# Kernel optimization log

Hardware: AMD Instinct MI355X
Metric: run time of the kernel (lower is better)

Reference implementation:

```python
import jax, jax.numpy as jnp
import numpy as np

NG, NR, C = 50000, 12000, 128     # lane nodes, roi nodes, n_map
NS = 6                            # num_scales
EPS, ELR, E1, E2 = 50000, 5000, 150000, 150000
GN_EPS = 1e-5


def gn(x, sb):
    # GroupNorm(num_groups=1) on [N, C]: normalize over C per row (biased var)
    m = x.mean(-1, keepdims=True)
    v = x.var(-1, keepdims=True)
    return (x - m) / jnp.sqrt(v + GN_EPS) * sb[0] + sb[1]


def lane_pooling(ctx_feat, ctx_pose, tgt_feat, tgt_pose, hi, wi,
                 input_w, relpose_w, relpose_b, ctx1_w, ctx1_gn, ctx2_w,
                 mlp1_w, mlp1_gn, mlp2_w, mlp2_gn, norm_gn):
    dist_feat = jax.nn.relu((ctx_pose[hi] - tgt_pose[wi]) @ relpose_w.T + relpose_b)  # [E,128]
    ctx = jnp.concatenate([ctx_feat[hi], dist_feat], -1)                               # [E,256]
    ctx = jax.nn.relu(gn(ctx @ ctx1_w.T, ctx1_gn)) @ ctx2_w.T                          # [E,128]
    identity = tgt_feat
    t = tgt_feat @ input_w.T
    t = t.at[wi].add(ctx)                 # scatter-reduce onto target nodes
    t = jax.nn.relu(gn(t, norm_gn))
    t = jax.nn.relu(gn(t @ mlp1_w.T, mlp1_gn))
    t = gn(t @ mlp2_w.T, mlp2_gn)
    return jax.nn.relu(t + identity)


def global_graph(feat, ps_u, ps_v, lr_u, lr_v,
                 ctr_w, ps_w, left_w, right_w, norm_gn, ctr2_w, ctr2_gn):
    res = feat
    for i in range(4):  # 4 fusion layers (structurally distinct weights)
        temp = feat @ ctr_w[i].T
        for k in range(2 * NS):  # pre0..pre5, suc0..suc5
            temp = temp.at[ps_u[k]].add(feat[ps_v[k]] @ ps_w[i, k].T)
        temp = temp.at[lr_u[0]].add(feat[lr_v[0]] @ left_w[i].T)
        temp = temp.at[lr_u[1]].add(feat[lr_v[1]] @ right_w[i].T)
        feat = jax.nn.relu(gn(temp, norm_gn[i]))
        feat = gn(feat @ ctr2_w[i].T, ctr2_gn[i])
        feat = jax.nn.relu(feat + res)
        res = feat
    return feat


def _gn_pack(key, lead):
    k1, k2 = jax.random.split(key)
    scale = 1.0 + 0.1 * jax.random.normal(k1, lead + (C,), jnp.float32)
    bias = 0.1 * jax.random.normal(k2, lead + (C,), jnp.float32)
    return jnp.stack([scale, bias], axis=-2)  # [..., 2, C]


def setup_inputs() -> dict:
    key = jax.random.key(0)
    ks = jax.random.split(key, 32)
    w = lambda k, sh: 0.05 * jax.random.normal(k, sh, jnp.float32)
    inp = {
        'roi_feat': jax.random.normal(ks[0], (NR, C), jnp.float32),
        'graph_pose': jax.random.normal(ks[1], (NG, 4), jnp.float32),
        'roi_pose': jax.random.normal(ks[2], (NR, 4), jnp.float32),
        'lp_input_w': w(ks[3], (2, C, C)),
        'lp_relpose_w': w(ks[4], (2, C, 4)),
        'lp_relpose_b': w(ks[5], (2, C)),
        'lp_ctx1_w': w(ks[6], (2, C, 2 * C)),
        'lp_ctx1_gn': _gn_pack(ks[7], (2,)),
        'lp_ctx2_w': w(ks[8], (2, C, C)),
        'lp_mlp1_w': w(ks[9], (2, C, C)),
        'lp_mlp1_gn': _gn_pack(ks[10], (2,)),
        'lp_mlp2_w': w(ks[11], (2, C, C)),
        'lp_mlp2_gn': _gn_pack(ks[12], (2,)),
        'lp_norm_gn': _gn_pack(ks[13], (2,)),
        'fuse_ctr_w': w(ks[14], (4, C, C)),
        'fuse_ps_w': w(ks[15], (4, 2 * NS, C, C)),
        'fuse_left_w': w(ks[16], (4, C, C)),
        'fuse_right_w': w(ks[17], (4, C, C)),
        'fuse_norm_gn': _gn_pack(ks[18], (4,)),
        'fuse_ctr2_w': w(ks[19], (4, C, C)),
        'fuse_ctr2_gn': _gn_pack(ks[20], (4,)),
        'e1_hi': jax.random.randint(ks[21], (E1,), 0, NR, jnp.int32),
        'e1_wi': jax.random.randint(ks[22], (E1,), 0, NG, jnp.int32),
        'e2_hi': jax.random.randint(ks[23], (E2,), 0, NG, jnp.int32),
        'e2_wi': jax.random.randint(ks[24], (E2,), 0, NR, jnp.int32),
        'ps_u': jax.random.randint(ks[25], (2 * NS, EPS), 0, NG, jnp.int32),
        'ps_v': jax.random.randint(ks[26], (2 * NS, EPS), 0, NG, jnp.int32),
        'lr_u': jax.random.randint(ks[27], (2, ELR), 0, NG, jnp.int32),
        'lr_v': jax.random.randint(ks[28], (2, ELR), 0, NG, jnp.int32),
    }
    return inp


def reference(roi_feat, graph_pose, roi_pose, lp_input_w, lp_relpose_w, lp_relpose_b,
              lp_ctx1_w, lp_ctx1_gn, lp_ctx2_w, lp_mlp1_w, lp_mlp1_gn, lp_mlp2_w,
              lp_mlp2_gn, lp_norm_gn, fuse_ctr_w, fuse_ps_w, fuse_left_w, fuse_right_w,
              fuse_norm_gn, fuse_ctr2_w, fuse_ctr2_gn, e1_hi, e1_wi, e2_hi, e2_wi,
              ps_u, ps_v, lr_u, lr_v):
    lp = lambda j: (lp_input_w[j], lp_relpose_w[j], lp_relpose_b[j], lp_ctx1_w[j],
                    lp_ctx1_gn[j], lp_ctx2_w[j], lp_mlp1_w[j], lp_mlp1_gn[j],
                    lp_mlp2_w[j], lp_mlp2_gn[j], lp_norm_gn[j])
    graph_feat = jnp.zeros((NG, C), jnp.float32)
    # roi2graph: context = roi, target = graph
    graph_feat = lane_pooling(roi_feat, roi_pose, graph_feat, graph_pose, e1_hi, e1_wi, *lp(0))
    graph_feat = global_graph(graph_feat, ps_u, ps_v, lr_u, lr_v,
                              fuse_ctr_w, fuse_ps_w, fuse_left_w, fuse_right_w,
                              fuse_norm_gn, fuse_ctr2_w, fuse_ctr2_gn)
    # graph2roi: context = graph, target = roi
    out = lane_pooling(graph_feat, graph_pose, roi_feat, roi_pose, e2_hi, e2_wi, *lp(1))
    return out
```

## Files before the change

### kernel.cpp

```cpp
#include <hip/hip_runtime.h>

#define NG 50000
#define NR 12000
#define EPS_N 50000
#define ELR_N 5000
#define E1_N 150000
#define E2_N 150000
#define GN_EPS_F 1e-5f
#define SCAN_CHUNK 4096
#define AST 136

typedef __attribute__((ext_vector_type(8))) __bf16 bf16x8;
typedef __attribute__((ext_vector_type(4))) float f32x4;

__device__ __forceinline__ bf16x8 cvt8(const float* __restrict__ p) {
    float4 x0 = *reinterpret_cast<const float4*>(p);
    float4 x1 = *reinterpret_cast<const float4*>(p + 4);
    bf16x8 a;
    a[0] = (__bf16)x0.x; a[1] = (__bf16)x0.y; a[2] = (__bf16)x0.z; a[3] = (__bf16)x0.w;
    a[4] = (__bf16)x1.x; a[5] = (__bf16)x1.y; a[6] = (__bf16)x1.z; a[7] = (__bf16)x1.w;
    return a;
}

struct PrepTab { const float* src[80]; int stride[80]; int n; };

__global__ void prepw_k(PrepTab tab, __bf16* __restrict__ wbuf)
{
    int t = blockIdx.x * 256 + threadIdx.x;
    int w = t >> 11;
    if (w >= tab.n) return;
    int rr = t & 2047;
    int chunk = rr >> 6, l = rr & 63;
    int waveN = chunk >> 4, ks = (chunk >> 2) & 3, ni = chunk & 3;
    int c = waveN * 64 + ni * 16 + (l & 15);
    int kb = (ks * 4 + (l >> 4)) * 8;
    const float* s = tab.src[w] + (size_t)c * tab.stride[w] + kb;
    bf16x8 o;
    #pragma unroll
    for (int e = 0; e < 8; ++e) o[e] = (__bf16)s[e];
    *reinterpret_cast<bf16x8*>(wbuf + (size_t)w * 16384 + rr * 8) = o;
}

__global__ void hist14_k(const int* __restrict__ ps_u, const int* __restrict__ lr_u,
                         int* __restrict__ cnt)
{
    int t = blockIdx.x * 256 + threadIdx.x;
    const int total = 12 * EPS_N + 2 * ELR_N;
    if (t >= total) return;
    int k, u;
    if (t < 12 * EPS_N) { k = t / EPS_N; u = ps_u[t]; }
    else { int r = t - 12 * EPS_N; k = 12 + r / ELR_N; u = lr_u[r]; }
    atomicAdd(&cnt[k * NG + u], 1);
}

__global__ void fill14_k(const int* __restrict__ ps_u, const int* __restrict__ ps_v,
                         const int* __restrict__ lr_u, const int* __restrict__ lr_v,
                         int* __restrict__ head, int* __restrict__ col)
{
    int t = blockIdx.x * 256 + threadIdx.x;
    const int total = 12 * EPS_N + 2 * ELR_N;
    if (t >= total) return;
    int k, u, v;
    if (t < 12 * EPS_N) { k = t / EPS_N; u = ps_u[t]; v = ps_v[t]; }
    else { int r = t - 12 * EPS_N; k = 12 + r / ELR_N; u = lr_u[r]; v = lr_v[r]; }
    int pos = atomicAdd(&head[k * NG + u], 1);
    col[pos] = v;
}

__global__ void histE_k(const int* __restrict__ wi, int n, int* __restrict__ cnt)
{
    int t = blockIdx.x * 256 + threadIdx.x;
    if (t >= n) return;
    atomicAdd(&cnt[wi[t]], 1);
}

__global__ void fillE_k(const int* __restrict__ wi, int n,
                        int* __restrict__ head, int* __restrict__ col)
{
    int t = blockIdx.x * 256 + threadIdx.x;
    if (t >= n) return;
    int pos = atomicAdd(&head[wi[t]], 1);
    col[pos] = t;
}

__global__ void scan1_k(const int* __restrict__ in, int n, int* __restrict__ bsum)
{
    __shared__ int sm[4];
    int base = blockIdx.x * SCAN_CHUNK;
    int s = 0;
    for (int i = threadIdx.x; i < SCAN_CHUNK; i += 256) {
        int idx = base + i;
        s += (idx < n) ? in[idx] : 0;
    }
    #pragma unroll
    for (int off = 1; off < 64; off <<= 1) s += __shfl_xor(s, off);
    if ((threadIdx.x & 63) == 0) sm[threadIdx.x >> 6] = s;
    __syncthreads();
    if (threadIdx.x == 0) bsum[blockIdx.x] = sm[0] + sm[1] + sm[2] + sm[3];
}

__global__ void scan2_k(int* __restrict__ bsum, int nb)
{
    if (threadIdx.x == 0) {
        int acc = 0;
        for (int i = 0; i < nb; ++i) { int t = bsum[i]; bsum[i] = acc; acc += t; }
    }
}

__global__ void scan3_k(const int* __restrict__ in, int n,
                        const int* __restrict__ bsum, int* __restrict__ outp)
{
    __shared__ int sm[256];
    int base = blockIdx.x * SCAN_CHUNK;
    int loc[16]; int s = 0;
    #pragma unroll
    for (int i = 0; i < 16; ++i) {
        int idx = base + threadIdx.x * 16 + i;
        loc[i] = (idx < n) ? in[idx] : 0; s += loc[i];
    }
    sm[threadIdx.x] = s; __syncthreads();
    for (int off = 1; off < 256; off <<= 1) {
        int v = (threadIdx.x >= off) ? sm[threadIdx.x - off] : 0;
        __syncthreads();
        sm[threadIdx.x] += v;
        __syncthreads();
    }
    int tp = (threadIdx.x ? sm[threadIdx.x - 1] : 0) + bsum[blockIdx.x];
    #pragma unroll
    for (int i = 0; i < 16; ++i) {
        int idx = base + threadIdx.x * 16 + i;
        if (idx < n) outp[idx] = tp;
        tp += loc[i];
        if (idx == n - 1) outp[n] = tp;
    }
}

__device__ __forceinline__ void mfma_tile(f32x4 (&acc)[2][4], const __bf16* atile,
                                          const __bf16* __restrict__ gw,
                                          int waveN, int r16, int kq, int lane)
{
    const __bf16* gwb = gw + ((size_t)waveN << 13) + lane * 8;
    #pragma unroll
    for (int ks = 0; ks < 4; ++ks) {
        bf16x8 a[2], b[4];
        #pragma unroll
        for (int mi = 0; mi < 2; ++mi) {
            const int lr = mi * 16 + r16;
            a[mi] = *reinterpret_cast<const bf16x8*>(atile + lr * AST + ((ks << 2) + kq) * 8);
        }
        #pragma unroll
        for (int ni = 0; ni < 4; ++ni)
            b[ni] = *reinterpret_cast<const bf16x8*>(gwb + ((ks << 2) + ni) * 512);
        #pragma unroll
        for (int mi = 0; mi < 2; ++mi)
            #pragma unroll
            for (int ni = 0; ni < 4; ++ni)
                acc[mi][ni] = __builtin_amdgcn_mfma_f32_16x16x32_bf16(
                    a[mi], b[ni], acc[mi][ni], 0, 0, 0);
    }
}

__device__ __forceinline__ void gn_stats(const f32x4 (&acc)[2][4],
                                         float (*smS)[32], float (*smQ)[32],
                                         int waveN, int r16, int kq)
{
    #pragma unroll
    for (int mi = 0; mi < 2; ++mi) {
        #pragma unroll
        for (int reg = 0; reg < 4; ++reg) {
            float s = acc[mi][0][reg] + acc[mi][1][reg] + acc[mi][2][reg] + acc[mi][3][reg];
            float q = acc[mi][0][reg]*acc[mi][0][reg] + acc[mi][1][reg]*acc[mi][1][reg]
                    + acc[mi][2][reg]*acc[mi][2][reg] + acc[mi][3][reg]*acc[mi][3][reg];
            #pragma unroll
            for (int off = 1; off < 16; off <<= 1) {
                s += __shfl_xor(s, off);
                q += __shfl_xor(q, off);
            }
            if (r16 == 0) {
                int lr = mi * 16 + kq * 4 + reg;
                smS[waveN][lr] = s; smQ[waveN][lr] = q;
            }
        }
    }
}

template<typename CT>
__launch_bounds__(128, 3)
__global__ void edgefull_k(const int* __restrict__ hi_idx, const int* __restrict__ wi_idx,
                           const CT* __restrict__ ctxfeat,
                           const float* __restrict__ cpose, const float* __restrict__ tpose,
                           const float* __restrict__ rpw, const float* __restrict__ rpb,
                           const __bf16* __restrict__ wc1A, const __bf16* __restrict__ wc1B,
                           const float* __restrict__ sb,
                           __bf16* __restrict__ hout, int M)
{
    __shared__ __bf16 atile[32 * AST];
    __shared__ float rw[640];
    __shared__ float smS[2][32], smQ[2][32];
    const int tid = threadIdx.x, lane = tid & 63, waveN = tid >> 6;
    const int r16 = lane & 15, kq = lane >> 4;
    const int ublk = blockIdx.x * 32;

    for (int i = tid; i < 640; i += 128)
        rw[i] = (i < 512) ? rpw[i] : rpb[i - 512];

    float dl[2][4];
    #pragma unroll
    for (int mi = 0; mi < 2; ++mi) {
        int r = ublk + mi * 16 + r16;
        int e = r < M ? r : M - 1;
        int hi = hi_idx[e], wi = wi_idx[e];
        float4 cp = *reinterpret_cast<const float4*>(cpose + (size_t)hi * 4);
        float4 tp = *reinterpret_cast<const float4*>(tpose + (size_t)wi * 4);
        dl[mi][0] = cp.x - tp.x; dl[mi][1] = cp.y - tp.y;
        dl[mi][2] = cp.z - tp.z; dl[mi][3] = cp.w - tp.w;
    }

    {
        const int glr = tid >> 2, q = tid & 3;
        const int e = (ublk + glr) < M ? (ublk + glr) : M - 1;
        const int cr = hi_idx[e];
        const CT* sp = ctxfeat + (size_t)cr * 128 + q * 32;
        #pragma unroll
        for (int i = 0; i < 4; ++i) {
            bf16x8 h;
            if constexpr (sizeof(CT) == 4) h = cvt8((const float*)sp + i * 8);
            else h = *reinterpret_cast<const bf16x8*>((const __bf16*)sp + i * 8);
            *reinterpret_cast<bf16x8*>(atile + glr * AST + (q * 4 + i) * 8) = h;
        }
    }
    __syncthreads();

    f32x4 acc[2][4];
    #pragma unroll
    for (int mi = 0; mi < 2; ++mi)
        #pragma unroll
        for (int ni = 0; ni < 4; ++ni)
            acc[mi][ni] = (f32x4){0.f, 0.f, 0.f, 0.f};

    mfma_tile(acc, atile, wc1A, waveN, r16, kq, lane);

    {
        const __bf16* gwb = wc1B + ((size_t)waveN << 13) + lane * 8;
        #pragma unroll
        for (int ks = 0; ks < 4; ++ks) {
            bf16x8 a[2], b[4];
            #pragma unroll
            for (int mi = 0; mi < 2; ++mi) {
                #pragma unroll
                for (int i = 0; i < 8; ++i) {
                    const int k = ks * 32 + kq * 8 + i;
                    float4 w4 = *reinterpret_cast<const float4*>(&rw[k * 4]);
                    float d = fmaf(dl[mi][0], w4.x, fmaf(dl[mi][1], w4.y,
                              fmaf(dl[mi][2], w4.z, fmaf(dl[mi][3], w4.w, rw[512 + k]))));
                    a[mi][i] = (__bf16)fmaxf(d, 0.f);
                }
            }
            #pragma unroll
            for (int ni = 0; ni < 4; ++ni)
                b[ni] = *reinterpret_cast<const bf16x8*>(gwb + ((ks << 2) + ni) * 512);
            #pragma unroll
            for (int mi = 0; mi < 2; ++mi)
                #pragma unroll
                for (int ni = 0; ni < 4; ++ni)
                    acc[mi][ni] = __builtin_amdgcn_mfma_f32_16x16x32_bf16(
                        a[mi], b[ni], acc[mi][ni], 0, 0, 0);
        }
    }

    gn_stats(acc, smS, smQ, waveN, r16, kq);
    __syncthreads();

    #pragma unroll
    for (int mi = 0; mi < 2; ++mi) {
        #pragma unroll
        for (int reg = 0; reg < 4; ++reg) {
            const int lr = mi * 16 + kq * 4 + reg;
            const float S = smS[0][lr] + smS[1][lr];
            const float Q = smQ[0][lr] + smQ[1][lr];
            const float m = S * (1.f / 128.f);
            const float inv = rsqrtf(fmaxf(Q * (1.f / 128.f) - m * m, 0.f) + GN_EPS_F);
            const int crow = ublk + lr;
            if (crow < M) {
                __bf16* dp = hout + (size_t)crow * 128 + waveN * 64 + r16;
                #pragma unroll
                for (int ni = 0; ni < 4; ++ni) {
                    const int colc = waveN * 64 + ni * 16 + r16;
                    float y = (acc[mi][ni][reg] - m) * inv * sb[colc] + sb[128 + colc];
                    dp[ni * 16] = (__bf16)fmaxf(y, 0.f);
                }
            }
        }
    }
}

struct FW { const __bf16* w[16]; };

__launch_bounds__(128, 3)
__global__ void fusedlayer_k(const __bf16* __restrict__ feat,
                             const int* __restrict__ rp, const int* __restrict__ col,
                             FW fw, const float* __restrict__ gn1,
                             const float* __restrict__ gn2,
                             __bf16* __restrict__ outp, int M)
{
    __shared__ __bf16 atile[2][32 * AST];
    __shared__ float smS[2][32], smQ[2][32];
    const int tid = threadIdx.x, lane = tid & 63, waveN = tid >> 6;
    const int r16 = lane & 15, kq = lane >> 4;
    const int ublk = blockIdx.x * 32;
    const int glr = tid >> 2, q = tid & 3;
    const int grow = ublk + glr;
    const bool gv = grow < M;
    const int grc = gv ? grow : 0;

    int begs[14], degs[14], c0[14];
    #pragma unroll
    for (int j = 0; j < 14; ++j) {
        int b = 0, e = 0;
        if (gv) { b = rp[j * M + grow]; e = rp[j * M + grow + 1]; }
        begs[j] = b; degs[j] = e - b;
    }
    #pragma unroll
    for (int j = 0; j < 14; ++j)
        c0[j] = (degs[j] > 0) ? col[begs[j]] : 0;

    float ss[32];
    auto GATHER = [&](int jj) {
        #pragma unroll
        for (int i = 0; i < 32; ++i) ss[i] = 0.f;
        if (jj == 14) {
            const __bf16* sp = feat + (size_t)grc * 128 + q * 32;
            #pragma unroll
            for (int i = 0; i < 4; ++i) {
                bf16x8 h = *reinterpret_cast<const bf16x8*>(sp + i * 8);
                #pragma unroll
                for (int e = 0; e < 8; ++e) ss[i * 8 + e] = (float)h[e];
            }
        } else {
            const int d = degs[jj];
            if (d > 0) {
                const __bf16* sp = feat + (size_t)c0[jj] * 128 + q * 32;
                #pragma unroll
                for (int i = 0; i < 4; ++i) {
                    bf16x8 h = *reinterpret_cast<const bf16x8*>(sp + i * 8);
                    #pragma unroll
                    for (int e2 = 0; e2 < 8; ++e2) ss[i * 8 + e2] += (float)h[e2];
                }
            }
            for (int t2 = begs[jj] + 1; t2 < begs[jj] + d; ++t2) {
                const __bf16* sp = feat + (size_t)col[t2] * 128 + q * 32;
                #pragma unroll
                for (int i = 0; i < 4; ++i) {
                    bf16x8 h = *reinterpret_cast<const bf16x8*>(sp + i * 8);
                    #pragma unroll
                    for (int e2 = 0; e2 < 8; ++e2) ss[i * 8 + e2] += (float)h[e2];
                }
            }
        }
    };

    f32x4 acc[2][4];
    #pragma unroll
    for (int mi = 0; mi < 2; ++mi)
        #pragma unroll
        for (int ni = 0; ni < 4; ++ni)
            acc[mi][ni] = (f32x4){0.f, 0.f, 0.f, 0.f};

    GATHER(0);
    #pragma unroll
    for (int j = 0; j < 15; ++j) {
        __bf16* at = atile[j & 1];
        #pragma unroll
        for (int i = 0; i < 4; ++i) {
            bf16x8 o;
            #pragma unroll
            for (int e = 0; e < 8; ++e) o[e] = (__bf16)ss[i * 8 + e];
            *reinterpret_cast<bf16x8*>(at + glr * AST + (q * 4 + i) * 8) = o;
        }
        __syncthreads();
        if (j < 14) GATHER(j + 1);
        mfma_tile(acc, at, fw.w[j], waveN, r16, kq, lane);
    }

    gn_stats(acc, smS, smQ, waveN, r16, kq);
    __syncthreads();
    {
        __bf16* at = atile[1];
        #pragma unroll
        for (int mi = 0; mi < 2; ++mi) {
            #pragma unroll
            for (int reg = 0; reg < 4; ++reg) {
                const int lr = mi * 16 + kq * 4 + reg;
                const float S = smS[0][lr] + smS[1][lr];
                const float Q = smQ[0][lr] + smQ[1][lr];
                const float m = S * (1.f / 128.f);
                const float inv = rsqrtf(fmaxf(Q * (1.f / 128.f) - m * m, 0.f) + GN_EPS_F);
                #pragma unroll
                for (int ni = 0; ni < 4; ++ni) {
                    const int colc = waveN * 64 + ni * 16 + r16;
                    float y = (acc[mi][ni][reg] - m) * inv * gn1[colc] + gn1[128 + colc];
                    at[lr * AST + colc] = (__bf16)fmaxf(y, 0.f);
                }
            }
        }
    }
    __syncthreads();

    f32x4 acc2[2][4];
    #pragma unroll
    for (int mi = 0; mi < 2; ++mi)
        #pragma unroll
        for (int ni = 0; ni < 4; ++ni)
            acc2[mi][ni] = (f32x4){0.f, 0.f, 0.f, 0.f};
    mfma_tile(acc2, atile[1], fw.w[15], waveN, r16, kq, lane);

    gn_stats(acc2, smS, smQ, waveN, r16, kq);
    __syncthreads();
    #pragma unroll
    for (int mi = 0; mi < 2; ++mi) {
        #pragma unroll
        for (int reg = 0; reg < 4; ++reg) {
            const int lr = mi * 16 + kq * 4 + reg;
            const float S = smS[0][lr] + smS[1][lr];
            const float Q = smQ[0][lr] + smQ[1][lr];
            const float m = S * (1.f / 128.f);
            const float inv = rsqrtf(fmaxf(Q * (1.f / 128.f) - m * m, 0.f) + GN_EPS_F);
            const int crow = ublk + lr;
            if (crow < M) {
                __bf16* dp = outp + (size_t)crow * 128 + waveN * 64 + r16;
                const __bf16* rs = feat + (size_t)crow * 128 + waveN * 64 + r16;
                #pragma unroll
                for (int ni = 0; ni < 4; ++ni) {
                    const int colc = waveN * 64 + ni * 16 + r16;
                    float y = (acc2[mi][ni][reg] - m) * inv * gn2[colc] + gn2[128 + colc];
                    y += (float)rs[ni * 16];
                    dp[ni * 16] = (__bf16)fmaxf(y, 0.f);
                }
            }
        }
    }
}

template<bool LP2>
__launch_bounds__(128, 3)
__global__ void lptail_k(const __bf16* __restrict__ hsrc,
                         const int* __restrict__ rp, const int* __restrict__ col,
                         const float* __restrict__ roi,
                         const __bf16* __restrict__ wc2, const __bf16* __restrict__ winW,
                         const __bf16* __restrict__ wm1, const __bf16* __restrict__ wm2,
                         const float* __restrict__ ngn, const float* __restrict__ m1gn,
                         const float* __restrict__ m2gn,
                         void* __restrict__ outp, int M)
{
    __shared__ __bf16 atile[32 * AST];
    __shared__ float smS[2][32], smQ[2][32];
    const int tid = threadIdx.x, lane = tid & 63, waveN = tid >> 6;
    const int r16 = lane & 15, kq = lane >> 4;
    const int ublk = blockIdx.x * 32;
    const int glr = tid >> 2, q = tid & 3;
    const int grow = ublk + glr;
    const bool gv = grow < M;

    {
        float ss[32];
        #pragma unroll
        for (int i = 0; i < 32; ++i) ss[i] = 0.f;
        if (gv) {
            const int b = rp[grow], e = rp[grow + 1];
            for (int jj = b; jj < e; ++jj) {
                const __bf16* sp = hsrc + (size_t)col[jj] * 128 + q * 32;
                #pragma unroll
                for (int i = 0; i < 4; ++i) {
                    bf16x8 h = *reinterpret_cast<const bf16x8*>(sp + i * 8);
                    #pragma unroll
                    for (int e2 = 0; e2 < 8; ++e2) ss[i * 8 + e2] += (float)h[e2];
                }
            }
        }
        #pragma unroll
        for (int i = 0; i < 4; ++i) {
            bf16x8 o;
            #pragma unroll
            for (int e2 = 0; e2 < 8; ++e2) o[e2] = (__bf16)ss[i * 8 + e2];
            *reinterpret_cast<bf16x8*>(atile + glr * AST + (q * 4 + i) * 8) = o;
        }
    }
    __syncthreads();

    f32x4 acc[2][4];
    #pragma unroll
    for (int mi = 0; mi < 2; ++mi)
        #pragma unroll
        for (int ni = 0; ni < 4; ++ni)
            acc[mi][ni] = (f32x4){0.f, 0.f, 0.f, 0.f};
    mfma_tile(acc, atile, wc2, waveN, r16, kq, lane);

    if (LP2) {
        __syncthreads();
        {
            const float* sp = roi + (size_t)(gv ? grow : 0) * 128 + q * 32;
            #pragma unroll
            for (int i = 0; i < 4; ++i)
                *reinterpret_cast<bf16x8*>(atile + glr * AST + (q * 4 + i) * 8) =
                    cvt8(sp + i * 8);
        }
        __syncthreads();
        mfma_tile(acc, atile, winW, waveN, r16, kq, lane);
    }

    auto CHAIN = [&](const float* SBP, const __bf16* WNEXT) {
        gn_stats(acc, smS, smQ, waveN, r16, kq);
        __syncthreads();
        #pragma unroll
        for (int mi = 0; mi < 2; ++mi) {
            #pragma unroll
            for (int reg = 0; reg < 4; ++reg) {
                const int lr = mi * 16 + kq * 4 + reg;
                const float S = smS[0][lr] + smS[1][lr];
                const float Q = smQ[0][lr] + smQ[1][lr];
                const float m = S * (1.f / 128.f);
                const float inv = rsqrtf(fmaxf(Q * (1.f / 128.f) - m * m, 0.f) + GN_EPS_F);
                #pragma unroll
                for (int ni = 0; ni < 4; ++ni) {
                    const int colc = waveN * 64 + ni * 16 + r16;
                    float y = (acc[mi][ni][reg] - m) * inv * SBP[colc] + SBP[128 + colc];
                    atile[lr * AST + colc] = (__bf16)fmaxf(y, 0.f);
                }
            }
        }
        __syncthreads();
        #pragma unroll
        for (int mi = 0; mi < 2; ++mi)
            #pragma unroll
            for (int ni = 0; ni < 4; ++ni)
                acc[mi][ni] = (f32x4){0.f, 0.f, 0.f, 0.f};
        mfma_tile(acc, atile, WNEXT, waveN, r16, kq, lane);
    };
    CHAIN(ngn, wm1);
    CHAIN(m1gn, wm2);

    gn_stats(acc, smS, smQ, waveN, r16, kq);
    __syncthreads();
    #pragma unroll
    for (int mi = 0; mi < 2; ++mi) {
        #pragma unroll
        for (int reg = 0; reg < 4; ++reg) {
            const int lr = mi * 16 + kq * 4 + reg;
            const float S = smS[0][lr] + smS[1][lr];
            const float Q = smQ[0][lr] + smQ[1][lr];
            const float m = S * (1.f / 128.f);
            const float inv = rsqrtf(fmaxf(Q * (1.f / 128.f) - m * m, 0.f) + GN_EPS_F);
            const int crow = ublk + lr;
            if (crow < M) {
                #pragma unroll
                for (int ni = 0; ni < 4; ++ni) {
                    const int colc = waveN * 64 + ni * 16 + r16;
                    float y = (acc[mi][ni][reg] - m) * inv * m2gn[colc] + m2gn[128 + colc];
                    if (LP2) {
                        y += roi[(size_t)crow * 128 + colc];
                        ((float*)outp)[(size_t)crow * 128 + colc] = fmaxf(y, 0.f);
                    } else {
                        ((__bf16*)outp)[(size_t)crow * 128 + colc] = (__bf16)fmaxf(y, 0.f);
                    }
                }
            }
        }
    }
}

extern "C" void kernel_launch(void* const* d_in, const int* in_sizes, int n_in,
                              void* d_out, int out_size, void* d_ws, size_t ws_size,
                              hipStream_t stream)
{
    const float* roi_feat   = (const float*)d_in[0];
    const float* graph_pose = (const float*)d_in[1];
    const float* roi_pose   = (const float*)d_in[2];
    const float* lp_input_w = (const float*)d_in[3];
    const float* lp_rpw     = (const float*)d_in[4];
    const float* lp_rpb     = (const float*)d_in[5];
    const float* lp_c1w     = (const float*)d_in[6];
    const float* lp_c1gn    = (const float*)d_in[7];
    const float* lp_c2w     = (const float*)d_in[8];
    const float* lp_m1w     = (const float*)d_in[9];
    const float* lp_m1gn    = (const float*)d_in[10];
    const float* lp_m2w     = (const float*)d_in[11];
    const float* lp_m2gn    = (const float*)d_in[12];
    const float* lp_ngn     = (const float*)d_in[13];
    const float* f_ctrw     = (const float*)d_in[14];
    const float* f_psw      = (const float*)d_in[15];
    const float* f_lw       = (const float*)d_in[16];
    const float* f_rw       = (const float*)d_in[17];
    const float* f_ngn      = (const float*)d_in[18];
    const float* f_c2w      = (const float*)d_in[19];
    const float* f_c2gn     = (const float*)d_in[20];
    const int* e1_hi = (const int*)d_in[21];
    const int* e1_wi = (const int*)d_in[22];
    const int* e2_hi = (const int*)d_in[23];
    const int* e2_wi = (const int*)d_in[24];
    const int* ps_u  = (const int*)d_in[25];
    const int* ps_v  = (const int*)d_in[26];
    const int* lr_u  = (const int*)d_in[27];
    const int* lr_v  = (const int*)d_in[28];
    float* out = (float*)d_out;

    __bf16* gA   = (__bf16*)d_ws;
    __bf16* gB   = gA + (size_t)NG * 128;
    __bf16* hbuf = gB + (size_t)NG * 128;
    __bf16* wbuf = hbuf + (size_t)E1_N * 128;
    int* ip      = (int*)(wbuf + (size_t)80 * 16384);
    int* cnt14   = ip;             ip += 14 * NG;
    int* rp14    = ip;             ip += 14 * NG + 1;
    int* col14   = ip;             ip += 12 * EPS_N + 2 * ELR_N;
    int* cntE1   = ip;             ip += NG;
    int* rpE1    = ip;             ip += NG + 1;
    int* colE1   = ip;             ip += E1_N;
    int* cntE2   = ip;             ip += NR;
    int* rpE2    = ip;             ip += NR + 1;
    int* colE2   = ip;             ip += E2_N;
    int* bsum    = ip;             ip += 256;

    dim3 blk(256), blk128(128);
    const dim3 gNG32((NG + 31) / 32), gNR32((NR + 31) / 32), gE32((E1_N + 31) / 32);
    const int NE14 = 12 * EPS_N + 2 * ELR_N;
    const dim3 gH14((NE14 + 255) / 256);

    PrepTab tab; int nw = 0;
    auto addw = [&](const float* p, int s) { tab.src[nw] = p; tab.stride[nw] = s; ++nw; };
    addw(lp_c1w, 256);
    addw(lp_c1w + 128, 256);
    addw(lp_c1w + 32768, 256);
    addw(lp_c1w + 32768 + 128, 256);
    addw(lp_input_w + 16384, 128);
    addw(lp_c2w, 128); addw(lp_c2w + 16384, 128);
    addw(lp_m1w, 128); addw(lp_m1w + 16384, 128);
    addw(lp_m2w, 128); addw(lp_m2w + 16384, 128);
    for (int i = 0; i < 4; ++i) addw(f_ctrw + (size_t)i * 16384, 128);
    for (int i = 0; i < 4; ++i)
        for (int k = 0; k < 12; ++k) addw(f_psw + ((size_t)i * 12 + k) * 16384, 128);
    for (int i = 0; i < 4; ++i) addw(f_lw + (size_t)i * 16384, 128);
    for (int i = 0; i < 4; ++i) addw(f_rw + (size_t)i * 16384, 128);
    for (int i = 0; i < 4; ++i) addw(f_c2w + (size_t)i * 16384, 128);
    tab.n = nw;
    auto wb = [&](int idx) { return (const __bf16*)(wbuf + (size_t)idx * 16384); };
    prepw_k<<<dim3((nw * 2048 + 255) / 256), blk, 0, stream>>>(tab, wbuf);

    hipMemsetAsync(cnt14, 0, (size_t)14 * NG * 4, stream);
    hist14_k<<<gH14, blk, 0, stream>>>(ps_u, lr_u, cnt14);
    {
        int n = 14 * NG, nb = (n + SCAN_CHUNK - 1) / SCAN_CHUNK;
        scan1_k<<<nb, blk, 0, stream>>>(cnt14, n, bsum);
        scan2_k<<<1, blk, 0, stream>>>(bsum, nb);
        scan3_k<<<nb, blk, 0, stream>>>(cnt14, n, bsum, rp14);
    }
    hipMemcpyAsync(cnt14, rp14, (size_t)14 * NG * 4, hipMemcpyDeviceToDevice, stream);
    fill14_k<<<gH14, blk, 0, stream>>>(ps_u, ps_v, lr_u, lr_v, cnt14, col14);

    hipMemsetAsync(cntE1, 0, (size_t)NG * 4, stream);
    histE_k<<<(E1_N + 255) / 256, blk, 0, stream>>>(e1_wi, E1_N, cntE1);
    {
        int n = NG, nb = (n + SCAN_CHUNK - 1) / SCAN_CHUNK;
        scan1_k<<<nb, blk, 0, stream>>>(cntE1, n, bsum);
        scan2_k<<<1, blk, 0, stream>>>(bsum, nb);
        scan3_k<<<nb, blk, 0, stream>>>(cntE1, n, bsum, rpE1);
    }
    hipMemcpyAsync(cntE1, rpE1, (size_t)NG * 4, hipMemcpyDeviceToDevice, stream);
    fillE_k<<<(E1_N + 255) / 256, blk, 0, stream>>>(e1_wi, E1_N, cntE1, colE1);

    hipMemsetAsync(cntE2, 0, (size_t)NR * 4, stream);
    histE_k<<<(E2_N + 255) / 256, blk, 0, stream>>>(e2_wi, E2_N, cntE2);
    {
        int n = NR, nb = (n + SCAN_CHUNK - 1) / SCAN_CHUNK;
        scan1_k<<<nb, blk, 0, stream>>>(cntE2, n, bsum);
        scan2_k<<<1, blk, 0, stream>>>(bsum, nb);
        scan3_k<<<nb, blk, 0, stream>>>(cntE2, n, bsum, rpE2);
    }
    hipMemcpyAsync(cntE2, rpE2, (size_t)NR * 4, hipMemcpyDeviceToDevice, stream);
    fillE_k<<<(E2_N + 255) / 256, blk, 0, stream>>>(e2_wi, E2_N, cntE2, colE2);

    edgefull_k<float><<<gE32, blk128, 0, stream>>>(
        e1_hi, e1_wi, roi_feat, roi_pose, graph_pose, lp_rpw, lp_rpb,
        wb(0), wb(1), lp_c1gn, hbuf, E1_N);
    lptail_k<false><<<gNG32, blk128, 0, stream>>>(
        hbuf, rpE1, colE1, nullptr, wb(5), nullptr, wb(7), wb(9),
        lp_ngn, lp_m1gn, lp_m2gn, gA, NG);

    for (int i = 0; i < 4; ++i) {
        FW fw;
        for (int k = 0; k < 12; ++k) fw.w[k] = wb(15 + i * 12 + k);
        fw.w[12] = wb(63 + i); fw.w[13] = wb(67 + i);
        fw.w[14] = wb(11 + i); fw.w[15] = wb(71 + i);
        const __bf16* src = (i & 1) ? gB : gA;
        __bf16* dst = (i & 1) ? gA : gB;
        fusedlayer_k<<<gNG32, blk128, 0, stream>>>(
            src, rp14, col14, fw, f_ngn + (size_t)i * 256,
            f_c2gn + (size_t)i * 256, dst, NG);
    }

    edgefull_k<__bf16><<<gE32, blk128, 0, stream>>>(
        e2_hi, e2_wi, gA, graph_pose, roi_pose, lp_rpw + 512, lp_rpb + 128,
        wb(2), wb(3), lp_c1gn + 256, hbuf, E2_N);
    lptail_k<true><<<gNR32, blk128, 0, stream>>>(
        hbuf, rpE2, colE2, roi_feat, wb(6), wb(4), wb(8), wb(10),
        lp_ngn + 256, lp_m1gn + 256, lp_m2gn + 256, out, NR);
}
```

Measured before the change: 765.1 us.

## Give each wave a full 16x128 output tile and build MFMA fragments in registers

The work split changes from two waves sharing a 32-row tile (each owning 64 columns) to each wave owning 16 rows across all 128 columns. A-fragments are now gathered straight from global memory into registers in MFMA layout, and GroupNorm statistics are reduced within the wave by shuffles. This drops the shared-memory A tile, the cross-wave stat exchange and most block barriers. The cost is twice as many B-weight loads per wave (8 column fragments instead of 4), higher register pressure from 8 accumulators, and the loss of the software-pipelined gather that overlapped the next gather with the current MFMAs in the fusion kernel.

```diff
diff --git a/kernel.cpp b/kernel.cpp
--- a/kernel.cpp
+++ b/kernel.cpp
@@ -8,7 +8,7 @@
 #define E2_N 150000
 #define GN_EPS_F 1e-5f
 #define SCAN_CHUNK 4096
-#define AST 136
+#define WST 136
 
 typedef __attribute__((ext_vector_type(8))) __bf16 bf16x8;
 typedef __attribute__((ext_vector_type(4))) float f32x4;
@@ -31,8 +31,8 @@
     if (w >= tab.n) return;
     int rr = t & 2047;
     int chunk = rr >> 6, l = rr & 63;
-    int waveN = chunk >> 4, ks = (chunk >> 2) & 3, ni = chunk & 3;
-    int c = waveN * 64 + ni * 16 + (l & 15);
+    int wn = chunk >> 4, ks = (chunk >> 2) & 3, ni = chunk & 3;
+    int c = wn * 64 + ni * 16 + (l & 15);
     int kb = (ks * 4 + (l >> 4)) * 8;
     const float* s = tab.src[w] + (size_t)c * tab.stride[w] + kb;
     bf16x8 o;
@@ -135,53 +135,65 @@
     }
 }
 
-__device__ __forceinline__ void mfma_tile(f32x4 (&acc)[2][4], const __bf16* atile,
-                                          const __bf16* __restrict__ gw,
-                                          int waveN, int r16, int kq, int lane)
-{
-    const __bf16* gwb = gw + ((size_t)waveN << 13) + lane * 8;
+
+__device__ __forceinline__ void mfma16(f32x4 (&acc)[8], const bf16x8 (&a)[4],
+                                       const __bf16* __restrict__ gw, int lane)
+{
+    const __bf16* gwb = gw + lane * 8;
     #pragma unroll
     for (int ks = 0; ks < 4; ++ks) {
-        bf16x8 a[2], b[4];
-        #pragma unroll
-        for (int mi = 0; mi < 2; ++mi) {
-            const int lr = mi * 16 + r16;
-            a[mi] = *reinterpret_cast<const bf16x8*>(atile + lr * AST + ((ks << 2) + kq) * 8);
-        }
-        #pragma unroll
-        for (int ni = 0; ni < 4; ++ni)
-            b[ni] = *reinterpret_cast<const bf16x8*>(gwb + ((ks << 2) + ni) * 512);
-        #pragma unroll
-        for (int mi = 0; mi < 2; ++mi)
-            #pragma unroll
-            for (int ni = 0; ni < 4; ++ni)
-                acc[mi][ni] = __builtin_amdgcn_mfma_f32_16x16x32_bf16(
-                    a[mi], b[ni], acc[mi][ni], 0, 0, 0);
-    }
-}
-
-__device__ __forceinline__ void gn_stats(const f32x4 (&acc)[2][4],
-                                         float (*smS)[32], float (*smQ)[32],
-                                         int waveN, int r16, int kq)
-{
-    #pragma unroll
-    for (int mi = 0; mi < 2; ++mi) {
-        #pragma unroll
-        for (int reg = 0; reg < 4; ++reg) {
-            float s = acc[mi][0][reg] + acc[mi][1][reg] + acc[mi][2][reg] + acc[mi][3][reg];
-            float q = acc[mi][0][reg]*acc[mi][0][reg] + acc[mi][1][reg]*acc[mi][1][reg]
-                    + acc[mi][2][reg]*acc[mi][2][reg] + acc[mi][3][reg]*acc[mi][3][reg];
-            #pragma unroll
-            for (int off = 1; off < 16; off <<= 1) {
-                s += __shfl_xor(s, off);
-                q += __shfl_xor(q, off);
-            }
-            if (r16 == 0) {
-                int lr = mi * 16 + kq * 4 + reg;
-                smS[waveN][lr] = s; smQ[waveN][lr] = q;
-            }
-        }
-    }
+        #pragma unroll
+        for (int n2 = 0; n2 < 8; ++n2) {
+            const int chunk = (n2 >> 2) * 16 + ks * 4 + (n2 & 3);
+            bf16x8 b = *reinterpret_cast<const bf16x8*>(gwb + chunk * 512);
+            acc[n2] = __builtin_amdgcn_mfma_f32_16x16x32_bf16(a[ks], b, acc[n2], 0, 0, 0);
+        }
+    }
+}
+
+__device__ __forceinline__ void ss_to_frags(const float (&ss)[32], bf16x8 (&a)[4])
+{
+    #pragma unroll
+    for (int ks = 0; ks < 4; ++ks)
+        #pragma unroll
+        for (int i = 0; i < 8; ++i)
+            a[ks][i] = (__bf16)ss[ks * 8 + i];
+}
+
+__device__ __forceinline__ void gn_mi(const f32x4 (&acc)[8], float (&m)[4], float (&inv)[4])
+{
+    #pragma unroll
+    for (int reg = 0; reg < 4; ++reg) {
+        float s = 0.f, q = 0.f;
+        #pragma unroll
+        for (int n2 = 0; n2 < 8; ++n2) { float v = acc[n2][reg]; s += v; q = fmaf(v, v, q); }
+        #pragma unroll
+        for (int off = 1; off < 16; off <<= 1) {
+            s += __shfl_xor(s, off);
+            q += __shfl_xor(q, off);
+        }
+        m[reg] = s * (1.f / 128.f);
+        inv[reg] = rsqrtf(fmaxf(q * (1.f / 128.f) - m[reg] * m[reg], 0.f) + GN_EPS_F);
+    }
+}
+
+__device__ __forceinline__ void gn_relayout(const f32x4 (&acc)[8], const float* __restrict__ sb,
+                                            __bf16* wl, bf16x8 (&a)[4], int r16, int kq)
+{
+    float m[4], inv[4];
+    gn_mi(acc, m, inv);
+    #pragma unroll
+    for (int reg = 0; reg < 4; ++reg) {
+        #pragma unroll
+        for (int n2 = 0; n2 < 8; ++n2) {
+            const int colc = n2 * 16 + r16;
+            float y = (acc[n2][reg] - m[reg]) * inv[reg] * sb[colc] + sb[128 + colc];
+            wl[(kq * 4 + reg) * WST + colc] = (__bf16)fmaxf(y, 0.f);
+        }
+    }
+    #pragma unroll
+    for (int ks = 0; ks < 4; ++ks)
+        a[ks] = *reinterpret_cast<const bf16x8*>(wl + r16 * WST + ks * 32 + kq * 8);
 }
 
 template<typename CT>
@@ -194,101 +206,63 @@
                            const float* __restrict__ sb,
                            __bf16* __restrict__ hout, int M)
 {
-    __shared__ __bf16 atile[32 * AST];
     __shared__ float rw[640];
-    __shared__ float smS[2][32], smQ[2][32];
-    const int tid = threadIdx.x, lane = tid & 63, waveN = tid >> 6;
+    const int tid = threadIdx.x, lane = tid & 63, wv = tid >> 6;
     const int r16 = lane & 15, kq = lane >> 4;
-    const int ublk = blockIdx.x * 32;
+    const int wbase = blockIdx.x * 32 + wv * 16;
+    const int erow = wbase + r16;
+    const int ec = erow < M ? erow : M - 1;
 
     for (int i = tid; i < 640; i += 128)
         rw[i] = (i < 512) ? rpw[i] : rpb[i - 512];
-
-    float dl[2][4];
-    #pragma unroll
-    for (int mi = 0; mi < 2; ++mi) {
-        int r = ublk + mi * 16 + r16;
-        int e = r < M ? r : M - 1;
-        int hi = hi_idx[e], wi = wi_idx[e];
-        float4 cp = *reinterpret_cast<const float4*>(cpose + (size_t)hi * 4);
-        float4 tp = *reinterpret_cast<const float4*>(tpose + (size_t)wi * 4);
-        dl[mi][0] = cp.x - tp.x; dl[mi][1] = cp.y - tp.y;
-        dl[mi][2] = cp.z - tp.z; dl[mi][3] = cp.w - tp.w;
-    }
-
-    {
-        const int glr = tid >> 2, q = tid & 3;
-        const int e = (ublk + glr) < M ? (ublk + glr) : M - 1;
-        const int cr = hi_idx[e];
-        const CT* sp = ctxfeat + (size_t)cr * 128 + q * 32;
-        #pragma unroll
-        for (int i = 0; i < 4; ++i) {
-            bf16x8 h;
-            if constexpr (sizeof(CT) == 4) h = cvt8((const float*)sp + i * 8);
-            else h = *reinterpret_cast<const bf16x8*>((const __bf16*)sp + i * 8);
-            *reinterpret_cast<bf16x8*>(atile + glr * AST + (q * 4 + i) * 8) = h;
-        }
-    }
     __syncthreads();
 
-    f32x4 acc[2][4];
-    #pragma unroll
-    for (int mi = 0; mi < 2; ++mi)
-        #pragma unroll
-        for (int ni = 0; ni < 4; ++ni)
-            acc[mi][ni] = (f32x4){0.f, 0.f, 0.f, 0.f};
-
-    mfma_tile(acc, atile, wc1A, waveN, r16, kq, lane);
-
-    {
-        const __bf16* gwb = wc1B + ((size_t)waveN << 13) + lane * 8;
+    const int hi = hi_idx[ec], wi = wi_idx[ec];
+    float4 cp = *reinterpret_cast<const float4*>(cpose + (size_t)hi * 4);
+    float4 tp = *reinterpret_cast<const float4*>(tpose + (size_t)wi * 4);
+    const float d0 = cp.x - tp.x, d1 = cp.y - tp.y, d2 = cp.z - tp.z, d3 = cp.w - tp.w;
+
+    f32x4 acc[8];
+    #pragma unroll
+    for (int n2 = 0; n2 < 8; ++n2) acc[n2] = (f32x4){0.f, 0.f, 0.f, 0.f};
+
+    {
+        bf16x8 a[4];
+        const CT* sp = ctxfeat + (size_t)hi * 128 + kq * 8;
         #pragma unroll
         for (int ks = 0; ks < 4; ++ks) {
-            bf16x8 a[2], b[4];
+            if constexpr (sizeof(CT) == 4) a[ks] = cvt8((const float*)sp + ks * 32);
+            else a[ks] = *reinterpret_cast<const bf16x8*>((const __bf16*)sp + ks * 32);
+        }
+        mfma16(acc, a, wc1A, lane);
+    }
+    {
+        bf16x8 a[4];
+        #pragma unroll
+        for (int ks = 0; ks < 4; ++ks)
             #pragma unroll
-            for (int mi = 0; mi < 2; ++mi) {
-                #pragma unroll
-                for (int i = 0; i < 8; ++i) {
-                    const int k = ks * 32 + kq * 8 + i;
-                    float4 w4 = *reinterpret_cast<const float4*>(&rw[k * 4]);
-                    float d = fmaf(dl[mi][0], w4.x, fmaf(dl[mi][1], w4.y,
-                              fmaf(dl[mi][2], w4.z, fmaf(dl[mi][3], w4.w, rw[512 + k]))));
-                    a[mi][i] = (__bf16)fmaxf(d, 0.f);
-                }
-            }
+            for (int i = 0; i < 8; ++i) {
+                const int k = ks * 32 + kq * 8 + i;
+                float4 w4 = *reinterpret_cast<const float4*>(&rw[k * 4]);
+                float d = fmaf(d0, w4.x, fmaf(d1, w4.y, fmaf(d2, w4.z,
+                          fmaf(d3, w4.w, rw[512 + k]))));
+                a[ks][i] = (__bf16)fmaxf(d, 0.f);
+            }
+        mfma16(acc, a, wc1B, lane);
+    }
+
+    float m[4], inv[4];
+    gn_mi(acc, m, inv);
+    #pragma unroll
+    for (int reg = 0; reg < 4; ++reg) {
+        const int crow = wbase + kq * 4 + reg;
+        if (crow < M) {
+            __bf16* dp = hout + (size_t)crow * 128 + r16;
             #pragma unroll
-            for (int ni = 0; ni < 4; ++ni)
-                b[ni] = *reinterpret_cast<const bf16x8*>(gwb + ((ks << 2) + ni) * 512);
-            #pragma unroll
-            for (int mi = 0; mi < 2; ++mi)
-                #pragma unroll
-                for (int ni = 0; ni < 4; ++ni)
-                    acc[mi][ni] = __builtin_amdgcn_mfma_f32_16x16x32_bf16(
-                        a[mi], b[ni], acc[mi][ni], 0, 0, 0);
-        }
-    }
-
-    gn_stats(acc, smS, smQ, waveN, r16, kq);
-    __syncthreads();
-
-    #pragma unroll
-    for (int mi = 0; mi < 2; ++mi) {
-        #pragma unroll
-        for (int reg = 0; reg < 4; ++reg) {
-            const int lr = mi * 16 + kq * 4 + reg;
-            const float S = smS[0][lr] + smS[1][lr];
-            const float Q = smQ[0][lr] + smQ[1][lr];
-            const float m = S * (1.f / 128.f);
-            const float inv = rsqrtf(fmaxf(Q * (1.f / 128.f) - m * m, 0.f) + GN_EPS_F);
-            const int crow = ublk + lr;
-            if (crow < M) {
-                __bf16* dp = hout + (size_t)crow * 128 + waveN * 64 + r16;
-                #pragma unroll
-                for (int ni = 0; ni < 4; ++ni) {
-                    const int colc = waveN * 64 + ni * 16 + r16;
-                    float y = (acc[mi][ni][reg] - m) * inv * sb[colc] + sb[128 + colc];
-                    dp[ni * 16] = (__bf16)fmaxf(y, 0.f);
-                }
+            for (int n2 = 0; n2 < 8; ++n2) {
+                const int colc = n2 * 16 + r16;
+                float y = (acc[n2][reg] - m[reg]) * inv[reg] * sb[colc] + sb[128 + colc];
+                dp[n2 * 16] = (__bf16)fmaxf(y, 0.f);
             }
         }
     }
@@ -303,139 +277,67 @@
                              const float* __restrict__ gn2,
                              __bf16* __restrict__ outp, int M)
 {
-    __shared__ __bf16 atile[2][32 * AST];
-    __shared__ float smS[2][32], smQ[2][32];
-    const int tid = threadIdx.x, lane = tid & 63, waveN = tid >> 6;
+    __shared__ __bf16 wl[2][16 * WST];
+    const int tid = threadIdx.x, lane = tid & 63, wv = tid >> 6;
     const int r16 = lane & 15, kq = lane >> 4;
-    const int ublk = blockIdx.x * 32;
-    const int glr = tid >> 2, q = tid & 3;
-    const int grow = ublk + glr;
-    const bool gv = grow < M;
-    const int grc = gv ? grow : 0;
-
-    int begs[14], degs[14], c0[14];
-    #pragma unroll
-    for (int j = 0; j < 14; ++j) {
-        int b = 0, e = 0;
-        if (gv) { b = rp[j * M + grow]; e = rp[j * M + grow + 1]; }
-        begs[j] = b; degs[j] = e - b;
-    }
-    #pragma unroll
-    for (int j = 0; j < 14; ++j)
-        c0[j] = (degs[j] > 0) ? col[begs[j]] : 0;
-
-    float ss[32];
-    auto GATHER = [&](int jj) {
+    const int wbase = blockIdx.x * 32 + wv * 16;
+    const int wrow = (wbase + r16) < M ? (wbase + r16) : M - 1;
+
+    f32x4 acc[8];
+    #pragma unroll
+    for (int n2 = 0; n2 < 8; ++n2) acc[n2] = (f32x4){0.f, 0.f, 0.f, 0.f};
+
+    #pragma unroll
+    for (int j = 0; j < 15; ++j) {
+        float ss[32];
         #pragma unroll
         for (int i = 0; i < 32; ++i) ss[i] = 0.f;
-        if (jj == 14) {
-            const __bf16* sp = feat + (size_t)grc * 128 + q * 32;
+        if (j == 14) {
+            const __bf16* sp = feat + (size_t)wrow * 128 + kq * 8;
             #pragma unroll
-            for (int i = 0; i < 4; ++i) {
-                bf16x8 h = *reinterpret_cast<const bf16x8*>(sp + i * 8);
+            for (int ks = 0; ks < 4; ++ks) {
+                bf16x8 h = *reinterpret_cast<const bf16x8*>(sp + ks * 32);
                 #pragma unroll
-                for (int e = 0; e < 8; ++e) ss[i * 8 + e] = (float)h[e];
+                for (int i = 0; i < 8; ++i) ss[ks * 8 + i] = (float)h[i];
             }
         } else {
-            const int d = degs[jj];
-            if (d > 0) {
-                const __bf16* sp = feat + (size_t)c0[jj] * 128 + q * 32;
+            const int b = rp[j * M + wrow], e = rp[j * M + wrow + 1];
+            for (int t2 = b; t2 < e; ++t2) {
+                const __bf16* sp = feat + (size_t)col[t2] * 128 + kq * 8;
                 #pragma unroll
-                for (int i = 0; i < 4; ++i) {
-                    bf16x8 h = *reinterpret_cast<const bf16x8*>(sp + i * 8);
+                for (int ks = 0; ks < 4; ++ks) {
+                    bf16x8 h = *reinterpret_cast<const bf16x8*>(sp + ks * 32);
                     #pragma unroll
-                    for (int e2 = 0; e2 < 8; ++e2) ss[i * 8 + e2] += (float)h[e2];
+                    for (int i = 0; i < 8; ++i) ss[ks * 8 + i] += (float)h[i];
                 }
             }
-            for (int t2 = begs[jj] + 1; t2 < begs[jj] + d; ++t2) {
-                const __bf16* sp = feat + (size_t)col[t2] * 128 + q * 32;
-                #pragma unroll
-                for (int i = 0; i < 4; ++i) {
-                    bf16x8 h = *reinterpret_cast<const bf16x8*>(sp + i * 8);
-                    #pragma unroll
-                    for (int e2 = 0; e2 < 8; ++e2) ss[i * 8 + e2] += (float)h[e2];
-                }
-            }
-        }
-    };
-
-    f32x4 acc[2][4];
-    #pragma unroll
-    for (int mi = 0; mi < 2; ++mi)
-        #pragma unroll
-        for (int ni = 0; ni < 4; ++ni)
-            acc[mi][ni] = (f32x4){0.f, 0.f, 0.f, 0.f};
-
-    GATHER(0);
-    #pragma unroll
-    for (int j = 0; j < 15; ++j) {
-        __bf16* at = atile[j & 1];
-        #pragma unroll
-        for (int i = 0; i < 4; ++i) {
-            bf16x8 o;
+        }
+        bf16x8 a[4];
+        ss_to_frags(ss, a);
+        mfma16(acc, a, fw.w[j], lane);
+    }
+
+    bf16x8 a2[4];
+    gn_relayout(acc, gn1, wl[wv], a2, r16, kq);
+    f32x4 acc2[8];
+    #pragma unroll
+    for (int n2 = 0; n2 < 8; ++n2) acc2[n2] = (f32x4){0.f, 0.f, 0.f, 0.f};
+    mfma16(acc2, a2, fw.w[15], lane);
+
+    float m[4], inv[4];
+    gn_mi(acc2, m, inv);
+    #pragma unroll
+    for (int reg = 0; reg < 4; ++reg) {
+        const int crow = wbase + kq * 4 + reg;
+        if (crow < M) {
+            __bf16* dp = outp + (size_t)crow * 128 + r16;
+            const __bf16* rs = feat + (size_t)crow * 128 + r16;
             #pragma unroll
-            for (int e = 0; e < 8; ++e) o[e] = (__bf16)ss[i * 8 + e];
-            *reinterpret_cast<bf16x8*>(at + glr * AST + (q * 4 + i) * 8) = o;
-        }
-        __syncthreads();
-        if (j < 14) GATHER(j + 1);
-        mfma_tile(acc, at, fw.w[j], waveN, r16, kq, lane);
-    }
-
-    gn_stats(acc, smS, smQ, waveN, r16, kq);
-    __syncthreads();
-    {
-        __bf16* at = atile[1];
-        #pragma unroll
-        for (int mi = 0; mi < 2; ++mi) {
-            #pragma unroll
-            for (int reg = 0; reg < 4; ++reg) {
-                const int lr = mi * 16 + kq * 4 + reg;
-                const float S = smS[0][lr] + smS[1][lr];
-                const float Q = smQ[0][lr] + smQ[1][lr];
-                const float m = S * (1.f / 128.f);
-                const float inv = rsqrtf(fmaxf(Q * (1.f / 128.f) - m * m, 0.f) + GN_EPS_F);
-                #pragma unroll
-                for (int ni = 0; ni < 4; ++ni) {
-                    const int colc = waveN * 64 + ni * 16 + r16;
-                    float y = (acc[mi][ni][reg] - m) * inv * gn1[colc] + gn1[128 + colc];
-                    at[lr * AST + colc] = (__bf16)fmaxf(y, 0.f);
-                }
-            }
-        }
-    }
-    __syncthreads();
-
-    f32x4 acc2[2][4];
-    #pragma unroll
-    for (int mi = 0; mi < 2; ++mi)
-        #pragma unroll
-        for (int ni = 0; ni < 4; ++ni)
-            acc2[mi][ni] = (f32x4){0.f, 0.f, 0.f, 0.f};
-    mfma_tile(acc2, atile[1], fw.w[15], waveN, r16, kq, lane);
-
-    gn_stats(acc2, smS, smQ, waveN, r16, kq);
-    __syncthreads();
-    #pragma unroll
-    for (int mi = 0; mi < 2; ++mi) {
-        #pragma unroll
-        for (int reg = 0; reg < 4; ++reg) {
-            const int lr = mi * 16 + kq * 4 + reg;
-            const float S = smS[0][lr] + smS[1][lr];
-            const float Q = smQ[0][lr] + smQ[1][lr];
-            const float m = S * (1.f / 128.f);
-            const float inv = rsqrtf(fmaxf(Q * (1.f / 128.f) - m * m, 0.f) + GN_EPS_F);
-            const int crow = ublk + lr;
-            if (crow < M) {
-                __bf16* dp = outp + (size_t)crow * 128 + waveN * 64 + r16;
-                const __bf16* rs = feat + (size_t)crow * 128 + waveN * 64 + r16;
-                #pragma unroll
-                for (int ni = 0; ni < 4; ++ni) {
-                    const int colc = waveN * 64 + ni * 16 + r16;
-                    float y = (acc2[mi][ni][reg] - m) * inv * gn2[colc] + gn2[128 + colc];
-                    y += (float)rs[ni * 16];
-                    dp[ni * 16] = (__bf16)fmaxf(y, 0.f);
-                }
+            for (int n2 = 0; n2 < 8; ++n2) {
+                const int colc = n2 * 16 + r16;
+                float y = (acc2[n2][reg] - m[reg]) * inv[reg] * gn2[colc] + gn2[128 + colc];
+                y += (float)rs[n2 * 16];
+                dp[n2 * 16] = (__bf16)fmaxf(y, 0.f);
             }
         }
     }
@@ -452,116 +354,72 @@
                          const float* __restrict__ m2gn,
                          void* __restrict__ outp, int M)
 {
-    __shared__ __bf16 atile[32 * AST];
-    __shared__ float smS[2][32], smQ[2][32];
-    const int tid = threadIdx.x, lane = tid & 63, waveN = tid >> 6;
+    __shared__ __bf16 wl[2][16 * WST];
+    const int tid = threadIdx.x, lane = tid & 63, wv = tid >> 6;
     const int r16 = lane & 15, kq = lane >> 4;
-    const int ublk = blockIdx.x * 32;
-    const int glr = tid >> 2, q = tid & 3;
-    const int grow = ublk + glr;
-    const bool gv = grow < M;
+    const int wbase = blockIdx.x * 32 + wv * 16;
+    const int wrow = (wbase + r16) < M ? (wbase + r16) : M - 1;
+
+    f32x4 acc[8];
+    #pragma unroll
+    for (int n2 = 0; n2 < 8; ++n2) acc[n2] = (f32x4){0.f, 0.f, 0.f, 0.f};
 
     {
         float ss[32];
         #pragma unroll
         for (int i = 0; i < 32; ++i) ss[i] = 0.f;
-        if (gv) {
-            const int b = rp[grow], e = rp[grow + 1];
-            for (int jj = b; jj < e; ++jj) {
-                const __bf16* sp = hsrc + (size_t)col[jj] * 128 + q * 32;
+        const int b = rp[wrow], e = rp[wrow + 1];
+        for (int t2 = b; t2 < e; ++t2) {
+            const __bf16* sp = hsrc + (size_t)col[t2] * 128 + kq * 8;
+            #pragma unroll
+            for (int ks = 0; ks < 4; ++ks) {
+                bf16x8 h = *reinterpret_cast<const bf16x8*>(sp + ks * 32);
                 #pragma unroll
-                for (int i = 0; i < 4; ++i) {
-                    bf16x8 h = *reinterpret_cast<const bf16x8*>(sp + i * 8);
-                    #pragma unroll
-                    for (int e2 = 0; e2 < 8; ++e2) ss[i * 8 + e2] += (float)h[e2];
-                }
-            }
-        }
-        #pragma unroll
-        for (int i = 0; i < 4; ++i) {
-            bf16x8 o;
+                for (int i = 0; i < 8; ++i) ss[ks * 8 + i] += (float)h[i];
+            }
+        }
+        bf16x8 a[4];
+        ss_to_frags(ss, a);
+        mfma16(acc, a, wc2, lane);
+    }
+    if (LP2) {
+        bf16x8 a[4];
+        const float* sp = roi + (size_t)wrow * 128 + kq * 8;
+        #pragma unroll
+        for (int ks = 0; ks < 4; ++ks) a[ks] = cvt8(sp + ks * 32);
+        mfma16(acc, a, winW, lane);
+    }
+
+    {
+        bf16x8 a[4];
+        gn_relayout(acc, ngn, wl[wv], a, r16, kq);
+        #pragma unroll
+        for (int n2 = 0; n2 < 8; ++n2) acc[n2] = (f32x4){0.f, 0.f, 0.f, 0.f};
+        mfma16(acc, a, wm1, lane);
+    }
+    {
+        bf16x8 a[4];
+        gn_relayout(acc, m1gn, wl[wv], a, r16, kq);
+        #pragma unroll
+        for (int n2 = 0; n2 < 8; ++n2) acc[n2] = (f32x4){0.f, 0.f, 0.f, 0.f};
+        mfma16(acc, a, wm2, lane);
+    }
+
+    float m[4], inv[4];
+    gn_mi(acc, m, inv);
+    #pragma unroll
+    for (int reg = 0; reg < 4; ++reg) {
+        const int crow = wbase + kq * 4 + reg;
+        if (crow < M) {
             #pragma unroll
-            for (int e2 = 0; e2 < 8; ++e2) o[e2] = (__bf16)ss[i * 8 + e2];
-            *reinterpret_cast<bf16x8*>(atile + glr * AST + (q * 4 + i) * 8) = o;
-        }
-    }
-    __syncthreads();
-
-    f32x4 acc[2][4];
-    #pragma unroll
-    for (int mi = 0; mi < 2; ++mi)
-        #pragma unroll
-        for (int ni = 0; ni < 4; ++ni)
-            acc[mi][ni] = (f32x4){0.f, 0.f, 0.f, 0.f};
-    mfma_tile(acc, atile, wc2, waveN, r16, kq, lane);
-
-    if (LP2) {
-        __syncthreads();
-        {
-            const float* sp = roi + (size_t)(gv ? grow : 0) * 128 + q * 32;
-            #pragma unroll
-            for (int i = 0; i < 4; ++i)
-                *reinterpret_cast<bf16x8*>(atile + glr * AST + (q * 4 + i) * 8) =
-                    cvt8(sp + i * 8);
-        }
-        __syncthreads();
-        mfma_tile(acc, atile, winW, waveN, r16, kq, lane);
-    }
-
-    auto CHAIN = [&](const float* SBP, const __bf16* WNEXT) {
-        gn_stats(acc, smS, smQ, waveN, r16, kq);
-        __syncthreads();
-        #pragma unroll
-        for (int mi = 0; mi < 2; ++mi) {
-            #pragma unroll
-            for (int reg = 0; reg < 4; ++reg) {
-                const int lr = mi * 16 + kq * 4 + reg;
-                const float S = smS[0][lr] + smS[1][lr];
-                const float Q = smQ[0][lr] + smQ[1][lr];
-                const float m = S * (1.f / 128.f);
-                const float inv = rsqrtf(fmaxf(Q * (1.f / 128.f) - m * m, 0.f) + GN_EPS_F);
-                #pragma unroll
-                for (int ni = 0; ni < 4; ++ni) {
-                    const int colc = waveN * 64 + ni * 16 + r16;
-                    float y = (acc[mi][ni][reg] - m) * inv * SBP[colc] + SBP[128 + colc];
-                    atile[lr * AST + colc] = (__bf16)fmaxf(y, 0.f);
-                }
-            }
-        }
-        __syncthreads();
-        #pragma unroll
-        for (int mi = 0; mi < 2; ++mi)
-            #pragma unroll
-            for (int ni = 0; ni < 4; ++ni)
-                acc[mi][ni] = (f32x4){0.f, 0.f, 0.f, 0.f};
-        mfma_tile(acc, atile, WNEXT, waveN, r16, kq, lane);
-    };
-    CHAIN(ngn, wm1);
-    CHAIN(m1gn, wm2);
-
-    gn_stats(acc, smS, smQ, waveN, r16, kq);
-    __syncthreads();
-    #pragma unroll
-    for (int mi = 0; mi < 2; ++mi) {
-        #pragma unroll
-        for (int reg = 0; reg < 4; ++reg) {
-            const int lr = mi * 16 + kq * 4 + reg;
-            const float S = smS[0][lr] + smS[1][lr];
-            const float Q = smQ[0][lr] + smQ[1][lr];
-            const float m = S * (1.f / 128.f);
-            const float inv = rsqrtf(fmaxf(Q * (1.f / 128.f) - m * m, 0.f) + GN_EPS_F);
-            const int crow = ublk + lr;
-            if (crow < M) {
-                #pragma unroll
-                for (int ni = 0; ni < 4; ++ni) {
-                    const int colc = waveN * 64 + ni * 16 + r16;
-                    float y = (acc[mi][ni][reg] - m) * inv * m2gn[colc] + m2gn[128 + colc];
-                    if (LP2) {
-                        y += roi[(size_t)crow * 128 + colc];
-                        ((float*)outp)[(size_t)crow * 128 + colc] = fmaxf(y, 0.f);
-                    } else {
-                        ((__bf16*)outp)[(size_t)crow * 128 + colc] = (__bf16)fmaxf(y, 0.f);
-                    }
+            for (int n2 = 0; n2 < 8; ++n2) {
+                const int colc = n2 * 16 + r16;
+                float y = (acc[n2][reg] - m[reg]) * inv[reg] * m2gn[colc] + m2gn[128 + colc];
+                if (LP2) {
+                    y += roi[(size_t)crow * 128 + colc];
+                    ((float*)outp)[(size_t)crow * 128 + colc] = fmaxf(y, 0.f);
+                } else {
+                    ((__bf16*)outp)[(size_t)crow * 128 + colc] = (__bf16)fmaxf(y, 0.f);
                 }
             }
         }
```

New measurement: 697.3 us. -8.9%, faster.
